# Performance work log

Measured on AMD Instinct MI355X. Metric: run time of the kernel, lower is better.

The kernel has to match this reference:

```python
import jax, jax.numpy as jnp
import numpy as np

B, C, L, M, EMB, HID = 32, 64, 8192, 32, 256, 64

def setup_inputs() -> dict:
    key = jax.random.key(0)
    ks = jax.random.split(key, 14)
    s_w = 1.0 / (C * C)
    s_a = 1.0 / EMB
    return {
        "x": jax.random.normal(ks[0], (B, C, L), jnp.float32),
        "emb": jax.random.normal(ks[1], (B, EMB), jnp.float32),
        "weights_pos": s_w * jax.random.normal(ks[2], (C, C, M, 2), jnp.float32),
        "weights_neg": s_w * jax.random.normal(ks[3], (C, C, M, 2), jnp.float32),
        "A_real_pos": s_a * jax.random.normal(ks[4], (M, EMB), jnp.float32),
        "A_imag_pos": s_a * jax.random.normal(ks[5], (M, EMB), jnp.float32),
        "A_real_neg": s_a * jax.random.normal(ks[6], (M, EMB), jnp.float32),
        "A_imag_neg": s_a * jax.random.normal(ks[7], (M, EMB), jnp.float32),
        "tm_w1": 0.05 * jax.random.normal(ks[8], (HID, EMB), jnp.float32),
        "tm_b1": jnp.zeros((HID,), jnp.float32),
        "tm_w2": 0.05 * jax.random.normal(ks[9], (2 * C, HID), jnp.float32),
        "tm_b2": jnp.zeros((2 * C,), jnp.float32),
        "lin_w": 0.05 * jax.random.normal(ks[10], (C, C), jnp.float32),
        "lin_b": jnp.zeros((C,), jnp.float32),
    }

def reference(x, emb, weights_pos, weights_neg, A_real_pos, A_imag_pos,
              A_real_neg, A_imag_neg, tm_w1, tm_b1, tm_w2, tm_b2, lin_w, lin_b):
    b, c, l = x.shape
    m = weights_pos.shape[2]
    k = l // 2 + 1
    # ---- SpectralConv1d branch ----
    x_ft = jnp.fft.rfft(x, norm="ortho")  # [B,C,K] complex
    wp = weights_pos[..., 0] + 1j * weights_pos[..., 1]  # [Ci,Co,M]
    wn = weights_neg[..., 0] + 1j * weights_neg[..., 1]
    phi_p = (emb @ A_real_pos.T) + 1j * (emb @ A_imag_pos.T)  # [B,M]
    phi_n = (emb @ A_real_neg.T) + 1j * (emb @ A_imag_neg.T)
    out_pos = jnp.einsum("bim,iom->bom", x_ft[:, :, :m], wp) * phi_p[:, None, :]
    out_neg = jnp.einsum("bim,iom->bom", x_ft[:, :, k - m:], wn) * phi_n[:, None, :]
    out_ft = jnp.zeros((b, c, k), dtype=x_ft.dtype)
    out_ft = out_ft.at[:, :, :m].set(out_pos).at[:, :, k - m:].set(out_neg)
    x1 = jnp.fft.irfft(out_ft, n=l, norm="ortho")  # [B,C,L]
    # ---- Conv1DTime branch (FiLM-style) ----
    h = jax.nn.silu(emb @ tm_w1.T + tm_b1)          # [B,HID]
    gb = h @ tm_w2.T + tm_b2                         # [B,2C]
    gamma, beta = gb[:, :c], gb[:, c:]
    xl = jnp.einsum("bcl,oc->bol", x, lin_w) + lin_b[None, :, None]
    x2 = xl * (1.0 + gamma[:, :, None]) + beta[:, :, None]
    return jax.nn.silu(x1 + x2)
```

## Files before the change

kernel.cpp:

```cpp
#include <hip/hip_runtime.h>
#include <math.h>

#define L_ 8192
#define EMB_ 256
#define HID_ 64

typedef __attribute__((ext_vector_type(8))) short bf16x8;
typedef __attribute__((ext_vector_type(4))) float f32x4;
typedef __attribute__((ext_vector_type(4))) int i32x4;

#define OFF_TFB  0
#define OFF_TLB  262144
#define OFF_AFB  524288
#define OFF_XFRP 917504
#define OFF_AF   3014656
#define OFF_B2   3276800
#define OFF_PHI  3278848
#define OFF_GB   3282944

__device__ inline int pkbf(float a, float b) {
    int r;
    asm volatile("v_cvt_pk_bf16_f32 %0, %1, %2" : "=v"(r) : "v"(a), "v"(b));
    return r;
}
__device__ inline bf16x8 asbf(i32x4 v) { union { i32x4 i; bf16x8 h; } u; u.i = v; return u.h; }
#define MFMA(A,B,C) __builtin_amdgcn_mfma_f32_16x16x32_bf16((A),(B),(C),0,0,0)

__device__ inline ushort f2bf(float v) {
    unsigned b = __float_as_uint(v);
    return (ushort)((b + 0x7FFFu + ((b >> 16) & 1u)) >> 16);
}
__device__ inline float bf2f(ushort h) { return __uint_as_float(((unsigned)h) << 16); }
__device__ inline float lo16f(int h) { return __uint_as_float(((unsigned)h) << 16); }
__device__ inline float hi16f(int h) { return __uint_as_float(((unsigned)h) & 0xFFFF0000u); }

__global__ __launch_bounds__(256) void k_init(ushort* __restrict__ TLB, ushort* __restrict__ TFB,
        const float* __restrict__ emb,
        const float* __restrict__ Arp, const float* __restrict__ Aip,
        const float* __restrict__ Arn, const float* __restrict__ Ain, float* __restrict__ phi,
        const float* __restrict__ w1, const float* __restrict__ b1,
        const float* __restrict__ w2, const float* __restrict__ b2, float* __restrict__ gb) {
    int bid = blockIdx.x;
    if (bid < 4096) {
        int idx = bid * 256 + threadIdx.x;
        int f, l; ushort* dst;
        if (idx < 524288) {
            int u = idx;
            int e = u & 7, lane = (u >> 3) & 63, ct = (u >> 9) & 3, kstep = u >> 11;
            l = kstep * 32 + ((lane >> 4) << 3) + e;
            f = ct * 16 + (lane & 15);
            dst = TLB + u;
        } else {
            int u = idx - 524288;
            int e = u & 7, lane = (u >> 3) & 63, ts = (u >> 9) & 1, lt = u >> 10;
            l = lt * 16 + (lane & 15);
            f = ts * 32 + ((lane >> 4) << 3) + e;
            dst = TFB + u;
        }
        int fr = f & 31; bool sinp = (f & 32) != 0;
        int r = (fr * l) & (L_ - 1);
        float ang = (float)r * (6.283185307179586f / (float)L_);
        float v = sinp ? sinf(ang) : cosf(ang);
        *dst = f2bf(v);
    } else if (bid < 4112) {
        int tid = (bid - 4096) * 256 + threadIdx.x;
        int b = tid >> 7;
        int mm = (tid >> 2) & 31;
        int cmp = tid & 3;
        const float* A = (cmp == 0) ? Arp : (cmp == 1) ? Aip : (cmp == 2) ? Arn : Ain;
        const float4* e4 = (const float4*)(emb + b * EMB_);
        const float4* a4 = (const float4*)(A + mm * EMB_);
        float acc = 0.f;
        for (int q = 0; q < EMB_ / 4; ++q) {
            float4 ev = e4[q], av = a4[q];
            acc += ev.x * av.x + ev.y * av.y + ev.z * av.z + ev.w * av.w;
        }
        phi[tid] = acc;
    } else {
        __shared__ float h[HID_];
        int b = bid - 4112, t = threadIdx.x;
        if (t < HID_) {
            const float4* e4 = (const float4*)(emb + b * EMB_);
            const float4* w4 = (const float4*)(w1 + t * EMB_);
            float acc = b1[t];
            for (int q = 0; q < EMB_ / 4; ++q) {
                float4 ev = e4[q], wv = w4[q];
                acc += ev.x * wv.x + ev.y * wv.y + ev.z * wv.z + ev.w * wv.w;
            }
            h[t] = acc / (1.f + expf(-acc));
        }
        __syncthreads();
        if (t < 128) {
            float g = b2[t];
            const float4* h4 = (const float4*)h;
            const float4* w4 = (const float4*)(w2 + t * HID_);
            for (int q = 0; q < HID_ / 4; ++q) {
                float4 hv = h4[q], wv = w4[q];
                g += hv.x * wv.x + hv.y * wv.y + hv.z * wv.z + hv.w * wv.w;
            }
            if (t < 64) gb[(b * 64 + t) * 2 + 0] = 1.f + g;
            else        gb[(b * 64 + (t - 64)) * 2 + 1] = g;
        }
    }
}

__global__ __launch_bounds__(256) void k_dft(const float* __restrict__ x,
        const ushort* __restrict__ TLB, float* __restrict__ xfrp) {
    __shared__ float sP[4][16][132];
    int stripe = blockIdx.x >> 3;
    int lseg = blockIdx.x & 7;
    int w = threadIdx.x >> 6;
    int lane = threadIdx.x & 63;
    int row = lane & 15, koff = (lane >> 4) << 3;
    int r0 = stripe * 16;
    int kb0 = lseg * 1024 + w * 256;

    f32x4 acc[8];
    #pragma unroll
    for (int i = 0; i < 8; ++i) acc[i] = (f32x4){0.f, 0.f, 0.f, 0.f};

    const float* ap = x + (size_t)(r0 + row) * L_ + kb0 + koff;
    const i32x4* tb = (const i32x4*)TLB;
    int tbase = (kb0 >> 5) * 256 + lane;
    const i32x4 SM = {(int)0x80000000, (int)0x80000000, (int)0x80000000, (int)0x80000000};

    float4 xa0 = *(const float4*)(ap);
    float4 xc0 = *(const float4*)(ap + 4);
    float4 xa1 = *(const float4*)(ap + 32);
    float4 xc1 = *(const float4*)(ap + 36);
    for (int ks = 0; ks < 8; ++ks) {
        float4 nxa = {0,0,0,0}, nxc = {0,0,0,0};
        if (ks < 6) {
            nxa = *(const float4*)(ap + (ks + 2) * 32);
            nxc = *(const float4*)(ap + (ks + 2) * 32 + 4);
        }
        int h0 = pkbf(xa0.x, xa0.y), h1 = pkbf(xa0.z, xa0.w);
        int h2 = pkbf(xc0.x, xc0.y), h3 = pkbf(xc0.z, xc0.w);
        bf16x8 AH = asbf((i32x4){h0, h1, h2, h3});
        int tix = tbase + ks * 256;
        #pragma unroll
        for (int ct = 0; ct < 4; ++ct) {
            i32x4 bh = tb[tix + ct * 64];
            acc[ct] = MFMA(AH, asbf(bh), acc[ct]);
            acc[ct + 4] = MFMA(AH, asbf(bh ^ SM), acc[ct + 4]);
        }
        xa0 = xa1; xc0 = xc1; xa1 = nxa; xc1 = nxc;
    }
    int crow = (lane >> 4) << 2;
    int ccol = lane & 15;
    #pragma unroll
    for (int ct = 0; ct < 8; ++ct)
        #pragma unroll
        for (int r = 0; r < 4; ++r)
            sP[w][crow + r][ct * 16 + ccol] = acc[ct][r];
    __syncthreads();
    #pragma unroll
    for (int i = 0; i < 8; ++i) {
        int e = threadIdx.x + 256 * i;
        int rr = e & 15, cc = e >> 4;
        float s = sP[0][rr][cc] + sP[1][rr][cc] + sP[2][rr][cc] + sP[3][rr][cc];
        xfrp[((size_t)(lseg * 128 + cc)) * 2048 + r0 + rr] = s;
    }
}

__global__ __launch_bounds__(256) void k_mix(const float* __restrict__ xfrt,
        const float* __restrict__ wpos, const float* __restrict__ wneg,
        const float* __restrict__ phi, float* __restrict__ afull) {
    __shared__ float sW[64][64][2];
    __shared__ float sXr[16][64], sXi[16][64];
    int bi = blockIdx.x;
    int bh = bi & 1, side = (bi >> 1) & 1, mm = bi >> 2;
    int tid = threadIdx.x;
    int slot = side ? (31 - mm) : mm;
    int colR = side ? (64 + slot) : mm;
    int colI = side ? (96 + slot) : (32 + mm);

    const float* W = side ? wneg : wpos;
    #pragma unroll
    for (int j = 0; j < 16; ++j) {
        int fidx = tid + 256 * j;
        int i = fidx >> 6, o = fidx & 63;
        float2 wv = *(const float2*)&W[(size_t)(i * 64 + o) * 64 + mm * 2];
        sW[i][o][0] = wv.x;
        sW[i][o][1] = wv.y;
    }
    {
        const float4* pR = (const float4*)(xfrt + (size_t)colR * 2048 + bh * 1024);
        const float4* pI = (const float4*)(xfrt + (size_t)colI * 2048 + bh * 1024);
        float4 aR = {0, 0, 0, 0}, aI = {0, 0, 0, 0};
        #pragma unroll
        for (int s = 0; s < 8; ++s) {
            float4 vR = pR[(size_t)s * 65536 + tid];
            float4 vI = pI[(size_t)s * 65536 + tid];
            aR.x += vR.x; aR.y += vR.y; aR.z += vR.z; aR.w += vR.w;
            aI.x += vI.x; aI.y += vI.y; aI.z += vI.z; aI.w += vI.w;
        }
        if (!side) { aI.x = -aI.x; aI.y = -aI.y; aI.z = -aI.z; aI.w = -aI.w; }
        *(float4*)&sXr[tid >> 4][(tid & 15) * 4] = aR;
        *(float4*)&sXi[tid >> 4][(tid & 15) * 4] = aI;
    }
    __syncthreads();

    int o = tid & 63, bg = tid >> 6;
    const float invL = 1.f / (float)L_;
    float fac = (slot == 0) ? invL : 2.f * invL;
    int comp = side ? 2 : 0;
    #pragma unroll
    for (int bl = 0; bl < 4; ++bl) {
        int b_local = bg * 4 + bl;
        int b = bh * 16 + b_local;
        float sre = 0.f, sim = 0.f;
        #pragma unroll 16
        for (int i = 0; i < 64; ++i) {
            float wr = sW[i][o][0], wi = sW[i][o][1];
            float xr = sXr[b_local][i], xi = sXi[b_local][i];
            sre += xr * wr - xi * wi;
            sim += xr * wi + xi * wr;
        }
        const float* ph = &phi[(b * 32 + mm) * 4 + (side ? 2 : 0)];
        float phr = ph[0], phim = ph[1];
        float Pre = sre * phr - sim * phim;
        float Pim = sre * phim + sim * phr;
        float a = fac * Pre;
        float bcoef = (slot == 0) ? 0.f : (side ? 2.f * invL * Pim : -2.f * invL * Pim);
        afull[((size_t)b * 128 + comp * 32 + slot) * 64 + o] = a;
        afull[((size_t)b * 128 + (comp + 1) * 32 + slot) * 64 + o] = bcoef;
    }
}

__global__ __launch_bounds__(256) void k_folda(const float* __restrict__ lw,
        const float* __restrict__ lb, const float* __restrict__ gb,
        const float* __restrict__ af, ushort* __restrict__ afb, float* __restrict__ bias2) {
    int b = blockIdx.x, tid = threadIdx.x;
    const float* afs = af + (size_t)b * 128 * 64;
    ushort* dst = afb + (size_t)b * 24576;
    #pragma unroll
    for (int j = 0; j < 48; ++j) {
        int u = tid + 256 * j;
        int e = u & 7, lane = (u >> 3) & 63, mt = (u >> 9) & 3, ks = u >> 11;
        int c = mt * 16 + (lane & 15);
        int kk = ((lane >> 4) << 3) + e;
        float v = (ks < 4) ? afs[(ks * 32 + kk) * 64 + c]
                           : lw[c * 64 + (ks - 4) * 32 + kk] * gb[(b * 64 + c) * 2];
        ushort hi = f2bf(v);
        ushort lo = f2bf(v - bf2f(hi));
        int base = ((ks * 4 + mt) * 64 + lane) * 16;
        dst[base + e] = hi;
        dst[base + 8 + e] = lo;
    }
    if (tid < 64) {
        float g1 = gb[(b * 64 + tid) * 2], be = gb[(b * 64 + tid) * 2 + 1];
        bias2[b * 64 + tid] = lb[tid] * g1 + be;
    }
}

__global__ __launch_bounds__(256, 3) void k_fuse(const float* __restrict__ x,
        const ushort* __restrict__ TFB, const ushort* __restrict__ AFB,
        const float* __restrict__ bias2, float* __restrict__ out) {
    int b = blockIdx.x >> 6, lt = blockIdx.x & 63;
    int w = threadIdx.x >> 6, lane = threadIdx.x & 63;
    int col = lane & 15, kgrp = lane >> 4;
    int lbase = lt * 128 + w * 32;
    int lt0 = lbase >> 4;
    const i32x4* tb = (const i32x4*)TFB;
    const i32x4* ab = (const i32x4*)AFB + (size_t)b * 3072;

    f32x4 acc[4][2];
    #pragma unroll
    for (int i = 0; i < 4; ++i)
        #pragma unroll
        for (int j = 0; j < 2; ++j) acc[i][j] = (f32x4){0.f, 0.f, 0.f, 0.f};

    int sm = (col & 1) ? (int)0x80008000 : 0;
    i32x4 SM = {sm, sm, sm, sm};

    auto tpart = [&](int ts) {
        i32x4 bh[2];
        #pragma unroll
        for (int nj = 0; nj < 2; ++nj)
            bh[nj] = tb[((lt0 + nj) * 2 + ts) * 64 + lane];
        #pragma unroll
        for (int mt = 0; mt < 4; ++mt) {
            i32x4 ah0 = ab[((ts * 4 + mt) * 64 + lane) * 2];
            i32x4 ah1 = ab[(((2 + ts) * 4 + mt) * 64 + lane) * 2];
            bf16x8 AH0 = asbf(ah0), AH1 = asbf(ah1);
            #pragma unroll
            for (int nj = 0; nj < 2; ++nj) {
                acc[mt][nj] = MFMA(AH0, asbf(bh[nj]), acc[mt][nj]);
                acc[mt][nj] = MFMA(AH1, asbf(bh[nj] ^ SM), acc[mt][nj]);
            }
        }
    };
    auto xissue = [&](int ts, float xv[2][8]) {
        #pragma unroll
        for (int nj = 0; nj < 2; ++nj) {
            const float* xp = x + (size_t)(b * 64 + ts * 32 + kgrp * 8) * L_ + lbase + nj * 16 + col;
            #pragma unroll
            for (int e = 0; e < 8; ++e) xv[nj][e] = xp[(size_t)e * L_];
        }
    };
    auto xpart = [&](int ts, float xv[2][8]) {
        #pragma unroll
        for (int nj = 0; nj < 2; ++nj) {
            int h0 = pkbf(xv[nj][0], xv[nj][1]), h1 = pkbf(xv[nj][2], xv[nj][3]);
            int h2 = pkbf(xv[nj][4], xv[nj][5]), h3 = pkbf(xv[nj][6], xv[nj][7]);
            float r0 = xv[nj][0] - lo16f(h0), r1 = xv[nj][1] - hi16f(h0);
            float r2 = xv[nj][2] - lo16f(h1), r3 = xv[nj][3] - hi16f(h1);
            float r4 = xv[nj][4] - lo16f(h2), r5 = xv[nj][5] - hi16f(h2);
            float r6 = xv[nj][6] - lo16f(h3), r7 = xv[nj][7] - hi16f(h3);
            i32x4 xh = {h0, h1, h2, h3};
            i32x4 xl = {pkbf(r0, r1), pkbf(r2, r3), pkbf(r4, r5), pkbf(r6, r7)};
            bf16x8 XH = asbf(xh), XL = asbf(xl);
            #pragma unroll
            for (int mt = 0; mt < 4; ++mt) {
                int a = (((4 + ts) * 4 + mt) * 64 + lane) * 2;
                i32x4 ah = ab[a], al = ab[a + 1];
                bf16x8 AH = asbf(ah), AL = asbf(al);
                acc[mt][nj] = MFMA(AH, XH, acc[mt][nj]);
                acc[mt][nj] = MFMA(AL, XH, acc[mt][nj]);
                acc[mt][nj] = MFMA(AH, XL, acc[mt][nj]);
            }
        }
    };

    float xva[2][8], xvb[2][8];
    xissue(0, xva);
    tpart(0);
    xissue(1, xvb);
    xpart(0, xva);
    tpart(1);
    xpart(1, xvb);

    #pragma unroll
    for (int mt = 0; mt < 4; ++mt) {
        #pragma unroll
        for (int r = 0; r < 4; ++r) {
            int c = mt * 16 + kgrp * 4 + r;
            float bias = bias2[b * 64 + c];
            float* op = out + (size_t)(b * 64 + c) * L_ + lbase + col;
            #pragma unroll
            for (int nj = 0; nj < 2; ++nj) {
                float v = acc[mt][nj][r] + bias;
                op[nj * 16] = v / (1.f + __expf(-v));
            }
        }
    }
}

extern "C" void kernel_launch(void* const* d_in, const int* in_sizes, int n_in,
                              void* d_out, int out_size, void* d_ws, size_t ws_size,
                              hipStream_t stream) {
    const float* x    = (const float*)d_in[0];
    const float* emb  = (const float*)d_in[1];
    const float* wpos = (const float*)d_in[2];
    const float* wneg = (const float*)d_in[3];
    const float* Arp  = (const float*)d_in[4];
    const float* Aip  = (const float*)d_in[5];
    const float* Arn  = (const float*)d_in[6];
    const float* Ain  = (const float*)d_in[7];
    const float* w1   = (const float*)d_in[8];
    const float* b1   = (const float*)d_in[9];
    const float* w2   = (const float*)d_in[10];
    const float* b2   = (const float*)d_in[11];
    const float* lw   = (const float*)d_in[12];
    const float* lb   = (const float*)d_in[13];
    float* out = (float*)d_out;
    float* ws = (float*)d_ws;
    ushort* TFB  = (ushort*)(ws + OFF_TFB);
    ushort* TLB  = (ushort*)(ws + OFF_TLB);
    ushort* AFB  = (ushort*)(ws + OFF_AFB);
    float*  XFRP = ws + OFF_XFRP;
    float*  AF   = ws + OFF_AF;
    float*  B2   = ws + OFF_B2;
    float*  PHI  = ws + OFF_PHI;
    float*  GB   = ws + OFF_GB;

    hipLaunchKernelGGL(k_init,  dim3(4144), dim3(256), 0, stream,
                       TLB, TFB, emb, Arp, Aip, Arn, Ain, PHI, w1, b1, w2, b2, GB);
    hipLaunchKernelGGL(k_dft,   dim3(1024), dim3(256), 0, stream, x, TLB, XFRP);
    hipLaunchKernelGGL(k_mix,   dim3(128),  dim3(256), 0, stream, XFRP, wpos, wneg, PHI, AF);
    hipLaunchKernelGGL(k_folda, dim3(32),   dim3(256), 0, stream, lw, lb, GB, AF, AFB, B2);
    hipLaunchKernelGGL(k_fuse,  dim3(2048), dim3(256), 0, stream, x, TFB, AFB, B2, out);
}
```

Measured before the change: 82.54 us.

## Fuse folda into mix, deepen DFT prefetch, drop split-bf16 x correction

```diff
diff --git a/kernel.cpp b/kernel.cpp
--- a/kernel.cpp
+++ b/kernel.cpp
@@ -13,10 +13,9 @@
 #define OFF_TLB  262144
 #define OFF_AFB  524288
 #define OFF_XFRP 917504
-#define OFF_AF   3014656
-#define OFF_B2   3276800
-#define OFF_PHI  3278848
-#define OFF_GB   3282944
+#define OFF_B2   3014656
+#define OFF_PHI  3016704
+#define OFF_GB   3020800
 
 __device__ inline int pkbf(float a, float b) {
     int r;
@@ -31,8 +30,6 @@
     return (ushort)((b + 0x7FFFu + ((b >> 16) & 1u)) >> 16);
 }
 __device__ inline float bf2f(ushort h) { return __uint_as_float(((unsigned)h) << 16); }
-__device__ inline float lo16f(int h) { return __uint_as_float(((unsigned)h) << 16); }
-__device__ inline float hi16f(int h) { return __uint_as_float(((unsigned)h) & 0xFFFF0000u); }
 
 __global__ __launch_bounds__(256) void k_init(ushort* __restrict__ TLB, ushort* __restrict__ TFB,
         const float* __restrict__ emb,
@@ -128,23 +125,29 @@
     float4 xc0 = *(const float4*)(ap + 4);
     float4 xa1 = *(const float4*)(ap + 32);
     float4 xc1 = *(const float4*)(ap + 36);
+    float4 xa2 = *(const float4*)(ap + 64);
+    float4 xc2 = *(const float4*)(ap + 68);
+    i32x4 t0 = tb[tbase], t1 = tb[tbase + 64], t2 = tb[tbase + 128], t3 = tb[tbase + 192];
     for (int ks = 0; ks < 8; ++ks) {
         float4 nxa = {0,0,0,0}, nxc = {0,0,0,0};
-        if (ks < 6) {
-            nxa = *(const float4*)(ap + (ks + 2) * 32);
-            nxc = *(const float4*)(ap + (ks + 2) * 32 + 4);
+        i32x4 n0 = t0, n1 = t1, n2 = t2, n3 = t3;
+        if (ks < 5) {
+            nxa = *(const float4*)(ap + (ks + 3) * 32);
+            nxc = *(const float4*)(ap + (ks + 3) * 32 + 4);
+        }
+        if (ks < 7) {
+            int ti = tbase + (ks + 1) * 256;
+            n0 = tb[ti]; n1 = tb[ti + 64]; n2 = tb[ti + 128]; n3 = tb[ti + 192];
         }
         int h0 = pkbf(xa0.x, xa0.y), h1 = pkbf(xa0.z, xa0.w);
         int h2 = pkbf(xc0.x, xc0.y), h3 = pkbf(xc0.z, xc0.w);
         bf16x8 AH = asbf((i32x4){h0, h1, h2, h3});
-        int tix = tbase + ks * 256;
-        #pragma unroll
-        for (int ct = 0; ct < 4; ++ct) {
-            i32x4 bh = tb[tix + ct * 64];
-            acc[ct] = MFMA(AH, asbf(bh), acc[ct]);
-            acc[ct + 4] = MFMA(AH, asbf(bh ^ SM), acc[ct + 4]);
-        }
-        xa0 = xa1; xc0 = xc1; xa1 = nxa; xc1 = nxc;
+        acc[0] = MFMA(AH, asbf(t0), acc[0]); acc[4] = MFMA(AH, asbf(t0 ^ SM), acc[4]);
+        acc[1] = MFMA(AH, asbf(t1), acc[1]); acc[5] = MFMA(AH, asbf(t1 ^ SM), acc[5]);
+        acc[2] = MFMA(AH, asbf(t2), acc[2]); acc[6] = MFMA(AH, asbf(t2 ^ SM), acc[6]);
+        acc[3] = MFMA(AH, asbf(t3), acc[3]); acc[7] = MFMA(AH, asbf(t3 ^ SM), acc[7]);
+        xa0 = xa1; xc0 = xc1; xa1 = xa2; xc1 = xc2; xa2 = nxa; xc2 = nxc;
+        t0 = n0; t1 = n1; t2 = n2; t3 = n3;
     }
     int crow = (lane >> 4) << 2;
     int ccol = lane & 15;
@@ -165,12 +168,35 @@
 
 __global__ __launch_bounds__(256) void k_mix(const float* __restrict__ xfrt,
         const float* __restrict__ wpos, const float* __restrict__ wneg,
-        const float* __restrict__ phi, float* __restrict__ afull) {
+        const float* __restrict__ phi, const float* __restrict__ lw,
+        const float* __restrict__ lb, const float* __restrict__ gb,
+        ushort* __restrict__ afb, float* __restrict__ bias2) {
+    int bi = blockIdx.x;
+    int tid = threadIdx.x;
+    if (bi >= 128) {
+        int b = bi - 128;
+        ushort* dst = afb + (size_t)b * 24576;
+        #pragma unroll
+        for (int j = 0; j < 16; ++j) {
+            int u = tid + 256 * j;
+            int e = u & 7, lane = (u >> 3) & 63, mt = (u >> 9) & 3, ks2 = u >> 11;
+            int c = mt * 16 + (lane & 15);
+            int kk = ((lane >> 4) << 3) + e;
+            float v = lw[c * 64 + ks2 * 32 + kk] * gb[(b * 64 + c) * 2];
+            ushort hi = f2bf(v);
+            int base = (((4 + ks2) * 4 + mt) * 64 + lane) * 16;
+            dst[base + e] = hi;
+            dst[base + 8 + e] = f2bf(v - bf2f(hi));
+        }
+        if (tid < 64) {
+            float g1 = gb[(b * 64 + tid) * 2], be = gb[(b * 64 + tid) * 2 + 1];
+            bias2[b * 64 + tid] = lb[tid] * g1 + be;
+        }
+        return;
+    }
     __shared__ float sW[64][64][2];
     __shared__ float sXr[16][64], sXi[16][64];
-    int bi = blockIdx.x;
     int bh = bi & 1, side = (bi >> 1) & 1, mm = bi >> 2;
-    int tid = threadIdx.x;
     int slot = side ? (31 - mm) : mm;
     int colR = side ? (64 + slot) : mm;
     int colI = side ? (96 + slot) : (32 + mm);
@@ -205,6 +231,8 @@
     const float invL = 1.f / (float)L_;
     float fac = (slot == 0) ? invL : 2.f * invL;
     int comp = side ? 2 : 0;
+    int e = slot & 7, kgrp = slot >> 3;
+    int mt = o >> 4, lane = kgrp * 16 + (o & 15);
     #pragma unroll
     for (int bl = 0; bl < 4; ++bl) {
         int b_local = bg * 4 + bl;
@@ -223,34 +251,15 @@
         float Pim = sre * phim + sim * phr;
         float a = fac * Pre;
         float bcoef = (slot == 0) ? 0.f : (side ? 2.f * invL * Pim : -2.f * invL * Pim);
-        afull[((size_t)b * 128 + comp * 32 + slot) * 64 + o] = a;
-        afull[((size_t)b * 128 + (comp + 1) * 32 + slot) * 64 + o] = bcoef;
-    }
-}
-
-__global__ __launch_bounds__(256) void k_folda(const float* __restrict__ lw,
-        const float* __restrict__ lb, const float* __restrict__ gb,
-        const float* __restrict__ af, ushort* __restrict__ afb, float* __restrict__ bias2) {
-    int b = blockIdx.x, tid = threadIdx.x;
-    const float* afs = af + (size_t)b * 128 * 64;
-    ushort* dst = afb + (size_t)b * 24576;
-    #pragma unroll
-    for (int j = 0; j < 48; ++j) {
-        int u = tid + 256 * j;
-        int e = u & 7, lane = (u >> 3) & 63, mt = (u >> 9) & 3, ks = u >> 11;
-        int c = mt * 16 + (lane & 15);
-        int kk = ((lane >> 4) << 3) + e;
-        float v = (ks < 4) ? afs[(ks * 32 + kk) * 64 + c]
-                           : lw[c * 64 + (ks - 4) * 32 + kk] * gb[(b * 64 + c) * 2];
-        ushort hi = f2bf(v);
-        ushort lo = f2bf(v - bf2f(hi));
-        int base = ((ks * 4 + mt) * 64 + lane) * 16;
-        dst[base + e] = hi;
-        dst[base + 8 + e] = lo;
-    }
-    if (tid < 64) {
-        float g1 = gb[(b * 64 + tid) * 2], be = gb[(b * 64 + tid) * 2 + 1];
-        bias2[b * 64 + tid] = lb[tid] * g1 + be;
+        ushort* dst = afb + (size_t)b * 24576;
+        ushort hiA = f2bf(a);
+        int baseA = ((comp * 4 + mt) * 64 + lane) * 16;
+        dst[baseA + e] = hiA;
+        dst[baseA + 8 + e] = f2bf(a - bf2f(hiA));
+        ushort hiB = f2bf(bcoef);
+        int baseB = (((comp + 1) * 4 + mt) * 64 + lane) * 16;
+        dst[baseB + e] = hiB;
+        dst[baseB + 8 + e] = f2bf(bcoef - bf2f(hiB));
     }
 }
 
@@ -304,21 +313,11 @@
         for (int nj = 0; nj < 2; ++nj) {
             int h0 = pkbf(xv[nj][0], xv[nj][1]), h1 = pkbf(xv[nj][2], xv[nj][3]);
             int h2 = pkbf(xv[nj][4], xv[nj][5]), h3 = pkbf(xv[nj][6], xv[nj][7]);
-            float r0 = xv[nj][0] - lo16f(h0), r1 = xv[nj][1] - hi16f(h0);
-            float r2 = xv[nj][2] - lo16f(h1), r3 = xv[nj][3] - hi16f(h1);
-            float r4 = xv[nj][4] - lo16f(h2), r5 = xv[nj][5] - hi16f(h2);
-            float r6 = xv[nj][6] - lo16f(h3), r7 = xv[nj][7] - hi16f(h3);
-            i32x4 xh = {h0, h1, h2, h3};
-            i32x4 xl = {pkbf(r0, r1), pkbf(r2, r3), pkbf(r4, r5), pkbf(r6, r7)};
-            bf16x8 XH = asbf(xh), XL = asbf(xl);
+            bf16x8 XH = asbf((i32x4){h0, h1, h2, h3});
             #pragma unroll
             for (int mt = 0; mt < 4; ++mt) {
-                int a = (((4 + ts) * 4 + mt) * 64 + lane) * 2;
-                i32x4 ah = ab[a], al = ab[a + 1];
-                bf16x8 AH = asbf(ah), AL = asbf(al);
-                acc[mt][nj] = MFMA(AH, XH, acc[mt][nj]);
-                acc[mt][nj] = MFMA(AL, XH, acc[mt][nj]);
-                acc[mt][nj] = MFMA(AH, XL, acc[mt][nj]);
+                i32x4 ah = ab[(((4 + ts) * 4 + mt) * 64 + lane) * 2];
+                acc[mt][nj] = MFMA(asbf(ah), XH, acc[mt][nj]);
             }
         }
     };
@@ -370,7 +369,6 @@
     ushort* TLB  = (ushort*)(ws + OFF_TLB);
     ushort* AFB  = (ushort*)(ws + OFF_AFB);
     float*  XFRP = ws + OFF_XFRP;
-    float*  AF   = ws + OFF_AF;
     float*  B2   = ws + OFF_B2;
     float*  PHI  = ws + OFF_PHI;
     float*  GB   = ws + OFF_GB;
@@ -378,7 +376,7 @@
     hipLaunchKernelGGL(k_init,  dim3(4144), dim3(256), 0, stream,
                        TLB, TFB, emb, Arp, Aip, Arn, Ain, PHI, w1, b1, w2, b2, GB);
     hipLaunchKernelGGL(k_dft,   dim3(1024), dim3(256), 0, stream, x, TLB, XFRP);
-    hipLaunchKernelGGL(k_mix,   dim3(128),  dim3(256), 0, stream, XFRP, wpos, wneg, PHI, AF);
-    hipLaunchKernelGGL(k_folda, dim3(32),   dim3(256), 0, stream, lw, lb, GB, AF, AFB, B2);
+    hipLaunchKernelGGL(k_mix,   dim3(160),  dim3(256), 0, stream, XFRP, wpos, wneg, PHI,
+                       lw, lb, GB, AFB, B2);
     hipLaunchKernelGGL(k_fuse,  dim3(2048), dim3(256), 0, stream, x, TFB, AFB, B2, out);
 }
```

Result: faster. 72.49 us (-12.2%).
